# Kernel optimization log

Measured on AMD Instinct MI355X. Metric: run time of the kernel, lower is better.

## Reference

```python
import jax, jax.numpy as jnp
import numpy as np

B, T, D, H = 2, 2048, 1024, 16
DK = D // H


def setup_inputs() -> dict:
    key = jax.random.key(0)
    ks = jax.random.split(key, 9)
    s = 1.0 / np.sqrt(D)
    x = jax.random.normal(ks[0], (B, T, D), dtype=jnp.float32)
    # causal mask (1 = attend, 0 = masked), broadcast over batch and heads
    mask = jnp.tril(jnp.ones((T, T), dtype=jnp.int32))[None, None, :, :]
    Wq = jax.random.uniform(ks[1], (D, D), jnp.float32, -s, s)
    bq = jax.random.uniform(ks[2], (D,), jnp.float32, -s, s)
    Wk = jax.random.uniform(ks[3], (D, D), jnp.float32, -s, s)
    bk = jax.random.uniform(ks[4], (D,), jnp.float32, -s, s)
    Wv = jax.random.uniform(ks[5], (D, D), jnp.float32, -s, s)
    bv = jax.random.uniform(ks[6], (D,), jnp.float32, -s, s)
    Wo = jax.random.uniform(ks[7], (D, D), jnp.float32, -s, s)
    bo = jax.random.uniform(ks[8], (D,), jnp.float32, -s, s)
    return {"x": x, "mask": mask, "Wq": Wq, "bq": bq, "Wk": Wk, "bk": bk,
            "Wv": Wv, "bv": bv, "Wo": Wo, "bo": bo}


def reference(x, mask, Wq, bq, Wk, bk, Wv, bv, Wo, bo):
    # nn.Linear: y = x @ W.T + b
    q = (x @ Wq.T + bq).reshape(B, T, H, DK).transpose(0, 2, 1, 3)  # [B,H,T,DK]
    k = (x @ Wk.T + bk).reshape(B, T, H, DK).transpose(0, 2, 1, 3)
    v = (x @ Wv.T + bv).reshape(B, T, H, DK).transpose(0, 2, 1, 3)
    scores = jnp.einsum('bhqd,bhkd->bhqk', q, k) / np.sqrt(DK).astype(np.float32)
    scores = jnp.where(mask == 0, -jnp.inf, scores)
    attn = jax.nn.softmax(scores, axis=-1)
    out = jnp.einsum('bhqk,bhkd->bhqd', attn, v)  # [B,H,T,DK]
    out = out.transpose(0, 2, 1, 3).reshape(B, T, D)
    return out @ Wo.T + bo
```

## Files before the change

kernel.cpp:

```cpp
#include <hip/hip_runtime.h>

typedef unsigned short u16;
typedef unsigned long long u64;
typedef __attribute__((ext_vector_type(8))) short short8;
typedef __attribute__((ext_vector_type(4))) float f32x4;

#define B_ 2
#define T_ 2048
#define D_ 1024
#define H_ 16
#define DK_ 64

__device__ __forceinline__ u16 f2bf(float f){
  unsigned u = __float_as_uint(f);
  return (u16)((u + 0x7fffu + ((u >> 16) & 1u)) >> 16);
}

#if defined(__has_builtin)
#if __has_builtin(__builtin_amdgcn_global_load_lds)
#define HAS_GLLDS 1
#endif
#endif

#ifdef HAS_GLLDS
__device__ __forceinline__ void gl_lds16(const u16* g, u16* l){
  __builtin_amdgcn_global_load_lds(
      (__attribute__((address_space(1))) void*)(void*)g,
      (__attribute__((address_space(3))) void*)(void*)l, 16, 0, 0);
}
#endif

__global__ __launch_bounds__(256) void conv_x_k(const float* __restrict__ in,
                                                u16* __restrict__ out){
  int i = blockIdx.x * 256 + threadIdx.x;
  float4 v = ((const float4*)in)[i];
  u64 r = (u64)f2bf(v.x) | ((u64)f2bf(v.y) << 16) | ((u64)f2bf(v.z) << 32) | ((u64)f2bf(v.w) << 48);
  ((u64*)out)[i] = r;
}

__global__ __launch_bounds__(256) void conv_w_k(const float* w0, const float* w1,
                                                const float* w2, const float* w3,
                                                u16* o0, u16* o1, u16* o2, u16* o3){
  const float* src; u16* dst;
  switch (blockIdx.y){
    case 0: src = w0; dst = o0; break;
    case 1: src = w1; dst = o1; break;
    case 2: src = w2; dst = o2; break;
    default: src = w3; dst = o3; break;
  }
  int i = blockIdx.x * 256 + threadIdx.x;
  float4 v = ((const float4*)src)[i];
  u64 r = (u64)f2bf(v.x) | ((u64)f2bf(v.y) << 16) | ((u64)f2bf(v.z) << 32) | ((u64)f2bf(v.w) << 48);
  ((u64*)dst)[i] = r;
}

template<int NSEL, int OUT_F32>
__global__ __launch_bounds__(256) void gemm_bt_v2(
    const u16* __restrict__ A,
    const u16* __restrict__ W0, const u16* __restrict__ W1, const u16* __restrict__ W2,
    const float* __restrict__ b0, const float* __restrict__ b1, const float* __restrict__ b2,
    void* __restrict__ o0, void* __restrict__ o1, void* __restrict__ o2)
{
  __shared__ u16 As[128 * 32];
  __shared__ u16 Bs[128 * 32];
  const int tid = threadIdx.x;
  const int sel = (NSEL == 3) ? (blockIdx.x >> 3) : 0;
  const int n0 = (blockIdx.x & 7) * 128;
  const int m0 = blockIdx.y * 128;
  const u16* Bw = (sel == 0) ? W0 : ((sel == 1) ? W1 : W2);
  const float* bias = (sel == 0) ? b0 : ((sel == 1) ? b1 : b2);
  void* C = (sel == 0) ? o0 : ((sel == 1) ? o1 : o2);
  const int w = tid >> 6, l = tid & 63;
  const int lr = l & 15, lg = l >> 4;
  const int wm = (w & 1) * 64, wn = (w >> 1) * 64;
  f32x4 acc[4][4] = {};
  const u16* Ab = A  + (size_t)m0 * 1024;
  const u16* Bb = Bw + (size_t)n0 * 1024;
  for (int k0 = 0; k0 < 1024; k0 += 32){
    __syncthreads();
#ifdef HAS_GLLDS
#pragma unroll
    for (int i = 0; i < 2; ++i){
      int c = w * 2 + i;
      gl_lds16(Ab + (size_t)(16 * c + (l >> 2)) * 1024 + k0 + (l & 3) * 8, &As[c * 512]);
      gl_lds16(Bb + (size_t)(16 * c + (l >> 2)) * 1024 + k0 + (l & 3) * 8, &Bs[c * 512]);
    }
#else
#pragma unroll
    for (int p = 0; p < 2; ++p){
      int idx = p * 256 + tid; int row = idx >> 2; int cg = (idx & 3) * 8;
      *(uint4*)&As[row * 32 + cg] = *(const uint4*)(Ab + (size_t)row * 1024 + k0 + cg);
      *(uint4*)&Bs[row * 32 + cg] = *(const uint4*)(Bb + (size_t)row * 1024 + k0 + cg);
    }
#endif
    __syncthreads();
    short8 af[4], bfr[4];
#pragma unroll
    for (int mi = 0; mi < 4; ++mi) af[mi]  = *(const short8*)&As[(wm + 16 * mi + lr) * 32 + 8 * lg];
#pragma unroll
    for (int ni = 0; ni < 4; ++ni) bfr[ni] = *(const short8*)&Bs[(wn + 16 * ni + lr) * 32 + 8 * lg];
#pragma unroll
    for (int mi = 0; mi < 4; ++mi)
#pragma unroll
      for (int ni = 0; ni < 4; ++ni)
        acc[mi][ni] = __builtin_amdgcn_mfma_f32_16x16x32_bf16(af[mi], bfr[ni], acc[mi][ni], 0, 0, 0);
  }
  float bv[4];
#pragma unroll
  for (int ni = 0; ni < 4; ++ni) bv[ni] = bias[n0 + wn + 16 * ni + lr];
#pragma unroll
  for (int mi = 0; mi < 4; ++mi)
#pragma unroll
    for (int ni = 0; ni < 4; ++ni)
#pragma unroll
      for (int r = 0; r < 4; ++r){
        float v = acc[mi][ni][r] + bv[ni];
        size_t off = (size_t)(m0 + wm + 16 * mi + lg * 4 + r) * 1024 + (n0 + wn + 16 * ni + lr);
        if (OUT_F32) ((float*)C)[off] = v;
        else         ((u16*)C)[off]   = f2bf(v);
      }
}

__global__ __launch_bounds__(256) void transpose_v_k(const u16* __restrict__ V,
                                                     u16* __restrict__ VT){
  __shared__ u16 L[64 * 72];
  const int tid = threadIdx.x;
  const int tc = blockIdx.x, h = blockIdx.y, b = blockIdx.z;
#pragma unroll
  for (int p = 0; p < 2; ++p){
    int row = (tid >> 3) + 32 * p, g = tid & 7;
    *(uint4*)&L[row * 72 + g * 8] =
        *(const uint4*)(V + ((size_t)(b * T_ + tc * 64 + row) * H_ + h) * DK_ + g * 8);
  }
  __syncthreads();
#pragma unroll
  for (int p = 0; p < 2; ++p){
    int d = tid >> 2, g8 = (tid & 3) + 4 * p;
    union { uint4 u; u16 s[8]; } tv;
#pragma unroll
    for (int i = 0; i < 8; ++i){
      int pp = 8 * g8 + i;
      int tl = 16 * (pp & 3) + (pp >> 2);
      tv.s[i] = L[tl * 72 + d];
    }
    *(uint4*)(VT + ((size_t)(b * H_ + h) * DK_ + d) * T_ + tc * 64 + 8 * g8) = tv.u;
  }
}

#define AP 72
__global__ __launch_bounds__(256) void attn_v2(
    const u16* __restrict__ Q, const u16* __restrict__ K,
    const u16* __restrict__ VTp, u16* __restrict__ O)
{
  __shared__ u16 Ks[64 * AP];
  __shared__ u16 VTs[64 * AP];
  __shared__ u16 Ps[4][32 * AP];
  const int tid = threadIdx.x;
  const int w = tid >> 6, l = tid & 63;
  const int lr = l & 15, lg = l >> 4;
  const int h = blockIdx.y, b = blockIdx.z;
  const int qtb = (b == 0) ? blockIdx.x : (T_ / 128 - 1 - blockIdx.x);
  const int q0 = qtb * 128;
  const int wrow0 = q0 + w * 32;

  short8 qf[2][2];
#pragma unroll
  for (int mi = 0; mi < 2; ++mi)
#pragma unroll
    for (int s = 0; s < 2; ++s)
      qf[mi][s] = *(const short8*)(Q + ((size_t)(b * T_ + wrow0 + mi * 16 + lr) * H_ + h) * DK_ + s * 32 + lg * 8);

  f32x4 acc[2][4] = {};
  float lsum[2][4] = {};
  const int ktend = 2 * qtb + 1;
  const int srow = tid >> 3, sg = tid & 7;

  for (int kt = 0; kt <= ktend; ++kt){
    __syncthreads();
#pragma unroll
    for (int p = 0; p < 2; ++p){
      int row = srow + 32 * p;
      *(uint4*)&Ks[row * AP + sg * 8] =
          *(const uint4*)(K + ((size_t)(b * T_ + kt * 64 + row) * H_ + h) * DK_ + sg * 8);
      *(uint4*)&VTs[row * AP + sg * 8] =
          *(const uint4*)(VTp + ((size_t)(b * H_ + h) * DK_ + row) * T_ + kt * 64 + sg * 8);
    }
    __syncthreads();
    if (kt * 64 <= wrow0 + 31){
      short8 kf[4][2];
#pragma unroll
      for (int j0 = 0; j0 < 4; ++j0)
#pragma unroll
        for (int s = 0; s < 2; ++s)
          kf[j0][s] = *(const short8*)&Ks[(j0 * 16 + lr) * AP + s * 32 + 8 * lg];
      f32x4 sc[2][4];
#pragma unroll
      for (int mi = 0; mi < 2; ++mi)
#pragma unroll
        for (int j0 = 0; j0 < 4; ++j0){
          f32x4 z = {};
          z = __builtin_amdgcn_mfma_f32_16x16x32_bf16(qf[mi][0], kf[j0][0], z, 0, 0, 0);
          z = __builtin_amdgcn_mfma_f32_16x16x32_bf16(qf[mi][1], kf[j0][1], z, 0, 0, 0);
          sc[mi][j0] = z;
        }
      const bool domask = (kt * 64 + 63 > wrow0);
      const int kcol0 = kt * 64;
#pragma unroll
      for (int mi = 0; mi < 2; ++mi)
#pragma unroll
        for (int r = 0; r < 4; ++r){
          const int qrow = wrow0 + mi * 16 + lg * 4 + r;
          u64 pv = 0; float ls = 0.f;
#pragma unroll
          for (int j0 = 0; j0 < 4; ++j0){
            float p = __expf(sc[mi][j0][r] * 0.125f);
            if (domask && (kcol0 + j0 * 16 + lr > qrow)) p = 0.f;
            ls += p;
            pv |= ((u64)f2bf(p)) << (16 * j0);
          }
          lsum[mi][r] += ls;
          *(u64*)&Ps[w][(mi * 16 + lg * 4 + r) * AP + 4 * lr] = pv;
        }
#pragma unroll
      for (int ks = 0; ks < 2; ++ks){
        short8 pf0 = *(const short8*)&Ps[w][(lr) * AP + 32 * ks + 8 * lg];
        short8 pf1 = *(const short8*)&Ps[w][(16 + lr) * AP + 32 * ks + 8 * lg];
#pragma unroll
        for (int d0 = 0; d0 < 4; ++d0){
          short8 vf = *(const short8*)&VTs[(d0 * 16 + lr) * AP + 32 * ks + 8 * lg];
          acc[0][d0] = __builtin_amdgcn_mfma_f32_16x16x32_bf16(pf0, vf, acc[0][d0], 0, 0, 0);
          acc[1][d0] = __builtin_amdgcn_mfma_f32_16x16x32_bf16(pf1, vf, acc[1][d0], 0, 0, 0);
        }
      }
    }
  }

#pragma unroll
  for (int mi = 0; mi < 2; ++mi)
#pragma unroll
    for (int r = 0; r < 4; ++r){
      float v = lsum[mi][r];
      v += __shfl_xor(v, 1); v += __shfl_xor(v, 2);
      v += __shfl_xor(v, 4); v += __shfl_xor(v, 8);
      lsum[mi][r] = v;
    }
#pragma unroll
  for (int mi = 0; mi < 2; ++mi)
#pragma unroll
    for (int d0 = 0; d0 < 4; ++d0)
#pragma unroll
      for (int r = 0; r < 4; ++r){
        float ov = acc[mi][d0][r] / lsum[mi][r];
        O[((size_t)(b * T_ + wrow0 + mi * 16 + lg * 4 + r) * H_ + h) * DK_ + d0 * 16 + lr] = f2bf(ov);
      }
}

extern "C" void kernel_launch(void* const* d_in, const int* in_sizes, int n_in,
                              void* d_out, int out_size, void* d_ws, size_t ws_size,
                              hipStream_t stream)
{
  const float* x  = (const float*)d_in[0];
  const float* Wq = (const float*)d_in[2];
  const float* bq = (const float*)d_in[3];
  const float* Wk = (const float*)d_in[4];
  const float* bk = (const float*)d_in[5];
  const float* Wv = (const float*)d_in[6];
  const float* bv = (const float*)d_in[7];
  const float* Wo = (const float*)d_in[8];
  const float* bo = (const float*)d_in[9];

  char* ws = (char*)d_ws;
  u16* xb  = (u16*)(ws + 0);
  u16* wqb = (u16*)(ws + 8388608);
  u16* wkb = (u16*)(ws + 10485760);
  u16* wvb = (u16*)(ws + 12582912);
  u16* wob = (u16*)(ws + 14680064);
  u16* qb  = (u16*)(ws + 16777216);
  u16* kb  = (u16*)(ws + 25165824);
  u16* vb  = (u16*)(ws + 33554432);
  u16* vtb = xb;
  u16* ab  = vb;

  conv_x_k<<<4096, 256, 0, stream>>>(x, xb);
  conv_w_k<<<dim3(1024, 4), 256, 0, stream>>>(Wq, Wk, Wv, Wo, wqb, wkb, wvb, wob);

  gemm_bt_v2<3, 0><<<dim3(24, 32), 256, 0, stream>>>(
      xb, wqb, wkb, wvb, bq, bk, bv, (void*)qb, (void*)kb, (void*)vb);

  transpose_v_k<<<dim3(T_ / 64, H_, B_), 256, 0, stream>>>(vb, vtb);

  attn_v2<<<dim3(T_ / 128, H_, B_), 256, 0, stream>>>(qb, kb, vtb, ab);

  gemm_bt_v2<1, 1><<<dim3(8, 32), 256, 0, stream>>>(
      ab, wob, wob, wob, bo, bo, bo, d_out, d_out, d_out);
}
```

Measured before the change: 141.3 us.

## Double-buffer GEMM and attention tiles, swizzle K/VT, fold softmax scale into Q

Both the GEMM and the attention kernels now double-buffer their LDS tiles, so the next tile's global-to-LDS load is issued before the current tile is computed, and each loop iteration needs one barrier instead of two. K and V^T are written with an XOR swizzle so attention can use unpadded LDS tiles without bank conflicts. The softmax scale times log2(e) is folded into Q in the projection epilogue, which lets attention use exp2 and packed bf16 conversion. The conversion kernels are merged into one launch, the final division becomes a reciprocal multiply, and launch bounds are raised. The costs are more LDS per block and swizzled layouts that every producer and consumer must agree on.

```diff
diff --git a/kernel.cpp b/kernel.cpp
--- a/kernel.cpp
+++ b/kernel.cpp
@@ -1,25 +1,38 @@
 #include <hip/hip_runtime.h>
 
 typedef unsigned short u16;
+typedef unsigned int u32;
 typedef unsigned long long u64;
 typedef __attribute__((ext_vector_type(8))) short short8;
 typedef __attribute__((ext_vector_type(4))) float f32x4;
 
 #define B_ 2
 #define T_ 2048
-#define D_ 1024
 #define H_ 16
 #define DK_ 64
+#define QSCALE 0.18033688011112042f
 
 __device__ __forceinline__ u16 f2bf(float f){
   unsigned u = __float_as_uint(f);
   return (u16)((u + 0x7fffu + ((u >> 16) & 1u)) >> 16);
 }
 
+__device__ __forceinline__ u32 cvtpk(float lo, float hi){
+  u32 r;
+  asm("v_cvt_pk_bf16_f32 %0, %1, %2" : "=v"(r) : "v"(lo), "v"(hi));
+  return r;
+}
+
 #if defined(__has_builtin)
 #if __has_builtin(__builtin_amdgcn_global_load_lds)
 #define HAS_GLLDS 1
 #endif
+#if __has_builtin(__builtin_amdgcn_exp2f)
+#define EXP2(x) __builtin_amdgcn_exp2f(x)
+#endif
+#endif
+#ifndef EXP2
+#define EXP2(x) __expf(0.69314718056f * (x))
 #endif
 
 #ifdef HAS_GLLDS
@@ -30,95 +43,106 @@
 }
 #endif
 
-__global__ __launch_bounds__(256) void conv_x_k(const float* __restrict__ in,
-                                                u16* __restrict__ out){
-  int i = blockIdx.x * 256 + threadIdx.x;
-  float4 v = ((const float4*)in)[i];
-  u64 r = (u64)f2bf(v.x) | ((u64)f2bf(v.y) << 16) | ((u64)f2bf(v.z) << 32) | ((u64)f2bf(v.w) << 48);
-  ((u64*)out)[i] = r;
-}
-
-__global__ __launch_bounds__(256) void conv_w_k(const float* w0, const float* w1,
-                                                const float* w2, const float* w3,
-                                                u16* o0, u16* o1, u16* o2, u16* o3){
-  const float* src; u16* dst;
-  switch (blockIdx.y){
-    case 0: src = w0; dst = o0; break;
-    case 1: src = w1; dst = o1; break;
-    case 2: src = w2; dst = o2; break;
-    default: src = w3; dst = o3; break;
-  }
-  int i = blockIdx.x * 256 + threadIdx.x;
-  float4 v = ((const float4*)src)[i];
-  u64 r = (u64)f2bf(v.x) | ((u64)f2bf(v.y) << 16) | ((u64)f2bf(v.z) << 32) | ((u64)f2bf(v.w) << 48);
-  ((u64*)dst)[i] = r;
-}
-
-template<int NSEL, int OUT_F32>
-__global__ __launch_bounds__(256) void gemm_bt_v2(
+__global__ __launch_bounds__(256) void conv_all(
+    const float* __restrict__ x, const float* __restrict__ wq, const float* __restrict__ wk,
+    const float* __restrict__ wv, const float* __restrict__ wo,
+    u16* __restrict__ xb, u16* __restrict__ wqb, u16* __restrict__ wkb,
+    u16* __restrict__ wvb, u16* __restrict__ wob)
+{
+  int gid = blockIdx.x * 256 + threadIdx.x;
+  const float* src; u16* dst; int off;
+  if (gid < 1048576){ src = x; dst = xb; off = gid; }
+  else {
+    int t = gid - 1048576; int s = t >> 18; off = t & 262143;
+    src = (s==0)?wq:((s==1)?wk:((s==2)?wv:wo));
+    dst = (s==0)?wqb:((s==1)?wkb:((s==2)?wvb:wob));
+  }
+  float4 v = ((const float4*)src)[off];
+  u64 r = (u64)f2bf(v.x) | ((u64)f2bf(v.y)<<16) | ((u64)f2bf(v.z)<<32) | ((u64)f2bf(v.w)<<48);
+  ((u64*)dst)[off] = r;
+}
+
+template<int QKV>
+__global__ __launch_bounds__(256, 3) void gemm_k3(
     const u16* __restrict__ A,
     const u16* __restrict__ W0, const u16* __restrict__ W1, const u16* __restrict__ W2,
     const float* __restrict__ b0, const float* __restrict__ b1, const float* __restrict__ b2,
     void* __restrict__ o0, void* __restrict__ o1, void* __restrict__ o2)
 {
-  __shared__ u16 As[128 * 32];
-  __shared__ u16 Bs[128 * 32];
+  __shared__ u16 As[2][128*32];
+  __shared__ u16 Bs[2][128*32];
   const int tid = threadIdx.x;
-  const int sel = (NSEL == 3) ? (blockIdx.x >> 3) : 0;
+  const int sel = QKV ? (blockIdx.x >> 3) : 0;
   const int n0 = (blockIdx.x & 7) * 128;
   const int m0 = blockIdx.y * 128;
-  const u16* Bw = (sel == 0) ? W0 : ((sel == 1) ? W1 : W2);
-  const float* bias = (sel == 0) ? b0 : ((sel == 1) ? b1 : b2);
-  void* C = (sel == 0) ? o0 : ((sel == 1) ? o1 : o2);
-  const int w = tid >> 6, l = tid & 63;
-  const int lr = l & 15, lg = l >> 4;
-  const int wm = (w & 1) * 64, wn = (w >> 1) * 64;
+  const u16* Bw = (sel==0)?W0:((sel==1)?W1:W2);
+  const float* bias = (sel==0)?b0:((sel==1)?b1:b2);
+  const int w = tid>>6, l = tid&63;
+  const int lr = l&15, lg = l>>4;
+  const int wm = (w&1)*64, wn = (w>>1)*64;
+  const u16* Ab = A  + (size_t)m0*1024 + (size_t)(l>>2)*1024 + (l&3)*8;
+  const u16* Bb = Bw + (size_t)n0*1024 + (size_t)(l>>2)*1024 + (l&3)*8;
   f32x4 acc[4][4] = {};
-  const u16* Ab = A  + (size_t)m0 * 1024;
-  const u16* Bb = Bw + (size_t)n0 * 1024;
-  for (int k0 = 0; k0 < 1024; k0 += 32){
+
+#define G_STAGE(k0, pb) do {                                                    \
+    _Pragma("unroll")                                                           \
+    for (int i_ = 0; i_ < 2; ++i_){                                             \
+      int c_ = w*2 + i_;                                                        \
+      G_STAGE_ONE(Ab, As, c_, k0, pb); G_STAGE_ONE(Bb, Bs, c_, k0, pb);         \
+    } } while(0)
+#ifdef HAS_GLLDS
+#define G_STAGE_ONE(SRC, DST, c_, k0, pb) \
+    gl_lds16(SRC + (size_t)(16*(c_))*1024 + (k0), &DST[pb][(c_)*512])
+#else
+#define G_STAGE_ONE(SRC, DST, c_, k0, pb) \
+    *(uint4*)&DST[pb][(c_)*512 + l*8] = *(const uint4*)(SRC + (size_t)(16*(c_))*1024 + (k0))
+#endif
+
+  G_STAGE(0, 0);
+  __syncthreads();
+  for (int it = 0; it < 32; ++it){
+    const int pb = it & 1;
+    if (it < 31) G_STAGE((it+1)*32, pb^1);
+    short8 af[4], bf[4];
+#pragma unroll
+    for (int mi=0;mi<4;++mi) af[mi] = *(const short8*)&As[pb][(wm+16*mi+lr)*32 + 8*lg];
+#pragma unroll
+    for (int ni=0;ni<4;++ni) bf[ni] = *(const short8*)&Bs[pb][(wn+16*ni+lr)*32 + 8*lg];
+#pragma unroll
+    for (int mi=0;mi<4;++mi)
+#pragma unroll
+      for (int ni=0;ni<4;++ni)
+        acc[mi][ni] = __builtin_amdgcn_mfma_f32_16x16x32_bf16(af[mi], bf[ni], acc[mi][ni], 0,0,0);
     __syncthreads();
-#ifdef HAS_GLLDS
-#pragma unroll
-    for (int i = 0; i < 2; ++i){
-      int c = w * 2 + i;
-      gl_lds16(Ab + (size_t)(16 * c + (l >> 2)) * 1024 + k0 + (l & 3) * 8, &As[c * 512]);
-      gl_lds16(Bb + (size_t)(16 * c + (l >> 2)) * 1024 + k0 + (l & 3) * 8, &Bs[c * 512]);
+  }
+
+  float bv[4];
+#pragma unroll
+  for (int ni=0;ni<4;++ni) bv[ni] = bias[n0+wn+16*ni+lr];
+  void* C = QKV ? ((sel==0)?o0:((sel==1)?o1:o2)) : o0;
+#pragma unroll
+  for (int mi=0;mi<4;++mi)
+#pragma unroll
+    for (int r=0;r<4;++r){
+      const int trow = m0 + wm + 16*mi + 4*lg + r;
+#pragma unroll
+      for (int ni=0;ni<4;++ni){
+        float v = acc[mi][ni][r] + bv[ni];
+        int n = n0 + wn + 16*ni + lr;
+        if (!QKV){
+          ((float*)C)[(size_t)trow*1024 + n] = v;
+        } else if (sel == 0){
+          ((u16*)C)[(size_t)trow*1024 + n] = f2bf(v * QSCALE);
+        } else if (sel == 1){
+          int nsw = (n & ~63) | ((n & 63) ^ ((trow & 7) << 3));
+          ((u16*)C)[(size_t)trow*1024 + nsw] = f2bf(v);
+        } else {
+          ((u16*)C)[(size_t)trow*1024 + n] = f2bf(v);
+        }
+      }
     }
-#else
-#pragma unroll
-    for (int p = 0; p < 2; ++p){
-      int idx = p * 256 + tid; int row = idx >> 2; int cg = (idx & 3) * 8;
-      *(uint4*)&As[row * 32 + cg] = *(const uint4*)(Ab + (size_t)row * 1024 + k0 + cg);
-      *(uint4*)&Bs[row * 32 + cg] = *(const uint4*)(Bb + (size_t)row * 1024 + k0 + cg);
-    }
-#endif
-    __syncthreads();
-    short8 af[4], bfr[4];
-#pragma unroll
-    for (int mi = 0; mi < 4; ++mi) af[mi]  = *(const short8*)&As[(wm + 16 * mi + lr) * 32 + 8 * lg];
-#pragma unroll
-    for (int ni = 0; ni < 4; ++ni) bfr[ni] = *(const short8*)&Bs[(wn + 16 * ni + lr) * 32 + 8 * lg];
-#pragma unroll
-    for (int mi = 0; mi < 4; ++mi)
-#pragma unroll
-      for (int ni = 0; ni < 4; ++ni)
-        acc[mi][ni] = __builtin_amdgcn_mfma_f32_16x16x32_bf16(af[mi], bfr[ni], acc[mi][ni], 0, 0, 0);
-  }
-  float bv[4];
-#pragma unroll
-  for (int ni = 0; ni < 4; ++ni) bv[ni] = bias[n0 + wn + 16 * ni + lr];
-#pragma unroll
-  for (int mi = 0; mi < 4; ++mi)
-#pragma unroll
-    for (int ni = 0; ni < 4; ++ni)
-#pragma unroll
-      for (int r = 0; r < 4; ++r){
-        float v = acc[mi][ni][r] + bv[ni];
-        size_t off = (size_t)(m0 + wm + 16 * mi + lg * 4 + r) * 1024 + (n0 + wn + 16 * ni + lr);
-        if (OUT_F32) ((float*)C)[off] = v;
-        else         ((u16*)C)[off]   = f2bf(v);
-      }
+#undef G_STAGE
+#undef G_STAGE_ONE
 }
 
 __global__ __launch_bounds__(256) void transpose_v_k(const u16* __restrict__ V,
@@ -143,116 +167,135 @@
       int tl = 16 * (pp & 3) + (pp >> 2);
       tv.s[i] = L[tl * 72 + d];
     }
-    *(uint4*)(VT + ((size_t)(b * H_ + h) * DK_ + d) * T_ + tc * 64 + 8 * g8) = tv.u;
-  }
-}
-
-#define AP 72
-__global__ __launch_bounds__(256) void attn_v2(
+    *(uint4*)(VT + ((size_t)(b * H_ + h) * DK_ + d) * T_ + tc * 64 + ((8 * g8) ^ ((d & 7) << 3))) = tv.u;
+  }
+}
+
+__global__ __launch_bounds__(256, 2) void attn_v3(
     const u16* __restrict__ Q, const u16* __restrict__ K,
-    const u16* __restrict__ VTp, u16* __restrict__ O)
+    const u16* __restrict__ VT, u16* __restrict__ O)
 {
-  __shared__ u16 Ks[64 * AP];
-  __shared__ u16 VTs[64 * AP];
-  __shared__ u16 Ps[4][32 * AP];
+  __shared__ u16 Ks[2][64*64];
+  __shared__ u16 VTs[2][64*64];
+  __shared__ u16 Ps[4][32*72];
   const int tid = threadIdx.x;
-  const int w = tid >> 6, l = tid & 63;
-  const int lr = l & 15, lg = l >> 4;
+  const int w = tid>>6, l = tid&63;
+  const int lr = l&15, lg = l>>4;
   const int h = blockIdx.y, b = blockIdx.z;
-  const int qtb = (b == 0) ? blockIdx.x : (T_ / 128 - 1 - blockIdx.x);
+  const int qtb = (b==0) ? blockIdx.x : (15 - blockIdx.x);
   const int q0 = qtb * 128;
-  const int wrow0 = q0 + w * 32;
+  const int wrow0 = q0 + w*32;
+  const int sl_r = l>>3, sl_c = (l&7)*8;
+  const size_t kbase = ((size_t)(b*T_) * H_ + h) * DK_;
+  const size_t vbase = (size_t)(b*H_ + h) * DK_ * (size_t)T_;
+
+#define A_STAGE(kt, pb) do {                                                       \
+    _Pragma("unroll")                                                              \
+    for (int p_=0;p_<2;++p_){                                                      \
+      int r0_ = 8*w + 32*p_;                                                       \
+      A_STAGE_K(kt, pb, r0_); A_STAGE_V(kt, pb, r0_);                              \
+    } } while(0)
+#ifdef HAS_GLLDS
+#define A_STAGE_K(kt, pb, r0_) \
+    gl_lds16(K  + kbase + (size_t)((kt)*64 + r0_ + sl_r)*1024 + sl_c, &Ks[pb][r0_*64])
+#define A_STAGE_V(kt, pb, r0_) \
+    gl_lds16(VT + vbase + (size_t)(r0_ + sl_r)*T_ + (kt)*64 + sl_c, &VTs[pb][r0_*64])
+#else
+#define A_STAGE_K(kt, pb, r0_) \
+    *(uint4*)&Ks[pb][(r0_+sl_r)*64 + sl_c] = *(const uint4*)(K + kbase + (size_t)((kt)*64 + r0_ + sl_r)*1024 + sl_c)
+#define A_STAGE_V(kt, pb, r0_) \
+    *(uint4*)&VTs[pb][(r0_+sl_r)*64 + sl_c] = *(const uint4*)(VT + vbase + (size_t)(r0_ + sl_r)*T_ + (kt)*64 + sl_c)
+#endif
 
   short8 qf[2][2];
 #pragma unroll
-  for (int mi = 0; mi < 2; ++mi)
-#pragma unroll
-    for (int s = 0; s < 2; ++s)
-      qf[mi][s] = *(const short8*)(Q + ((size_t)(b * T_ + wrow0 + mi * 16 + lr) * H_ + h) * DK_ + s * 32 + lg * 8);
+  for (int mi=0;mi<2;++mi)
+#pragma unroll
+    for (int s=0;s<2;++s)
+      qf[mi][s] = *(const short8*)(Q + kbase + (size_t)(wrow0 + 16*mi + lr)*1024 + s*32 + 8*lg);
 
   f32x4 acc[2][4] = {};
   float lsum[2][4] = {};
-  const int ktend = 2 * qtb + 1;
-  const int srow = tid >> 3, sg = tid & 7;
-
+  const int ktend = 2*qtb + 1;
+
+  A_STAGE(0, 0);
+  __syncthreads();
   for (int kt = 0; kt <= ktend; ++kt){
-    __syncthreads();
-#pragma unroll
-    for (int p = 0; p < 2; ++p){
-      int row = srow + 32 * p;
-      *(uint4*)&Ks[row * AP + sg * 8] =
-          *(const uint4*)(K + ((size_t)(b * T_ + kt * 64 + row) * H_ + h) * DK_ + sg * 8);
-      *(uint4*)&VTs[row * AP + sg * 8] =
-          *(const uint4*)(VTp + ((size_t)(b * H_ + h) * DK_ + row) * T_ + kt * 64 + sg * 8);
-    }
-    __syncthreads();
-    if (kt * 64 <= wrow0 + 31){
+    const int pb = kt & 1;
+    if (kt < ktend) A_STAGE(kt+1, pb^1);
+    if (kt*64 <= wrow0 + 31){
       short8 kf[4][2];
 #pragma unroll
-      for (int j0 = 0; j0 < 4; ++j0)
-#pragma unroll
-        for (int s = 0; s < 2; ++s)
-          kf[j0][s] = *(const short8*)&Ks[(j0 * 16 + lr) * AP + s * 32 + 8 * lg];
+      for (int j0=0;j0<4;++j0)
+#pragma unroll
+        for (int s=0;s<2;++s)
+          kf[j0][s] = *(const short8*)&Ks[pb][(j0*16+lr)*64 + (((4*s+lg) ^ (lr&7))<<3)];
       f32x4 sc[2][4];
 #pragma unroll
-      for (int mi = 0; mi < 2; ++mi)
-#pragma unroll
-        for (int j0 = 0; j0 < 4; ++j0){
+      for (int mi=0;mi<2;++mi)
+#pragma unroll
+        for (int j0=0;j0<4;++j0){
           f32x4 z = {};
-          z = __builtin_amdgcn_mfma_f32_16x16x32_bf16(qf[mi][0], kf[j0][0], z, 0, 0, 0);
-          z = __builtin_amdgcn_mfma_f32_16x16x32_bf16(qf[mi][1], kf[j0][1], z, 0, 0, 0);
+          z = __builtin_amdgcn_mfma_f32_16x16x32_bf16(qf[mi][0], kf[j0][0], z, 0,0,0);
+          z = __builtin_amdgcn_mfma_f32_16x16x32_bf16(qf[mi][1], kf[j0][1], z, 0,0,0);
           sc[mi][j0] = z;
         }
-      const bool domask = (kt * 64 + 63 > wrow0);
-      const int kcol0 = kt * 64;
-#pragma unroll
-      for (int mi = 0; mi < 2; ++mi)
-#pragma unroll
-        for (int r = 0; r < 4; ++r){
-          const int qrow = wrow0 + mi * 16 + lg * 4 + r;
-          u64 pv = 0; float ls = 0.f;
-#pragma unroll
-          for (int j0 = 0; j0 < 4; ++j0){
-            float p = __expf(sc[mi][j0][r] * 0.125f);
-            if (domask && (kcol0 + j0 * 16 + lr > qrow)) p = 0.f;
-            ls += p;
-            pv |= ((u64)f2bf(p)) << (16 * j0);
+      const bool diag = (kt*64 + 63 > wrow0);
+#pragma unroll
+      for (int mi=0;mi<2;++mi)
+#pragma unroll
+        for (int r=0;r<4;++r){
+          float p0,p1,p2,p3;
+          if (diag){
+            const int lim = wrow0 + 16*mi + 4*lg + r - kt*64;
+            p0 = (lr      <= lim) ? EXP2(sc[mi][0][r]) : 0.f;
+            p1 = (16+lr   <= lim) ? EXP2(sc[mi][1][r]) : 0.f;
+            p2 = (32+lr   <= lim) ? EXP2(sc[mi][2][r]) : 0.f;
+            p3 = (48+lr   <= lim) ? EXP2(sc[mi][3][r]) : 0.f;
+          } else {
+            p0 = EXP2(sc[mi][0][r]); p1 = EXP2(sc[mi][1][r]);
+            p2 = EXP2(sc[mi][2][r]); p3 = EXP2(sc[mi][3][r]);
           }
-          lsum[mi][r] += ls;
-          *(u64*)&Ps[w][(mi * 16 + lg * 4 + r) * AP + 4 * lr] = pv;
+          lsum[mi][r] += (p0+p1)+(p2+p3);
+          u64 pv = (u64)cvtpk(p0,p1) | ((u64)cvtpk(p2,p3) << 32);
+          *(u64*)&Ps[w][(16*mi+4*lg+r)*72 + 4*lr] = pv;
         }
 #pragma unroll
-      for (int ks = 0; ks < 2; ++ks){
-        short8 pf0 = *(const short8*)&Ps[w][(lr) * AP + 32 * ks + 8 * lg];
-        short8 pf1 = *(const short8*)&Ps[w][(16 + lr) * AP + 32 * ks + 8 * lg];
-#pragma unroll
-        for (int d0 = 0; d0 < 4; ++d0){
-          short8 vf = *(const short8*)&VTs[(d0 * 16 + lr) * AP + 32 * ks + 8 * lg];
-          acc[0][d0] = __builtin_amdgcn_mfma_f32_16x16x32_bf16(pf0, vf, acc[0][d0], 0, 0, 0);
-          acc[1][d0] = __builtin_amdgcn_mfma_f32_16x16x32_bf16(pf1, vf, acc[1][d0], 0, 0, 0);
+      for (int ks=0;ks<2;++ks){
+        short8 pf0 = *(const short8*)&Ps[w][lr*72      + 32*ks + 8*lg];
+        short8 pf1 = *(const short8*)&Ps[w][(16+lr)*72 + 32*ks + 8*lg];
+#pragma unroll
+        for (int d0=0;d0<4;++d0){
+          short8 vf = *(const short8*)&VTs[pb][(d0*16+lr)*64 + (((4*ks+lg) ^ (lr&7))<<3)];
+          acc[0][d0] = __builtin_amdgcn_mfma_f32_16x16x32_bf16(pf0, vf, acc[0][d0], 0,0,0);
+          acc[1][d0] = __builtin_amdgcn_mfma_f32_16x16x32_bf16(pf1, vf, acc[1][d0], 0,0,0);
         }
       }
     }
-  }
-
-#pragma unroll
-  for (int mi = 0; mi < 2; ++mi)
-#pragma unroll
-    for (int r = 0; r < 4; ++r){
+    __syncthreads();
+  }
+
+#pragma unroll
+  for (int mi=0;mi<2;++mi)
+#pragma unroll
+    for (int r=0;r<4;++r){
       float v = lsum[mi][r];
-      v += __shfl_xor(v, 1); v += __shfl_xor(v, 2);
-      v += __shfl_xor(v, 4); v += __shfl_xor(v, 8);
-      lsum[mi][r] = v;
+      v += __shfl_xor(v,1); v += __shfl_xor(v,2);
+      v += __shfl_xor(v,4); v += __shfl_xor(v,8);
+      lsum[mi][r] = 1.0f / v;
     }
 #pragma unroll
-  for (int mi = 0; mi < 2; ++mi)
-#pragma unroll
-    for (int d0 = 0; d0 < 4; ++d0)
-#pragma unroll
-      for (int r = 0; r < 4; ++r){
-        float ov = acc[mi][d0][r] / lsum[mi][r];
-        O[((size_t)(b * T_ + wrow0 + mi * 16 + lg * 4 + r) * H_ + h) * DK_ + d0 * 16 + lr] = f2bf(ov);
+  for (int mi=0;mi<2;++mi)
+#pragma unroll
+    for (int d0=0;d0<4;++d0)
+#pragma unroll
+      for (int r=0;r<4;++r){
+        float ov = acc[mi][d0][r] * lsum[mi][r];
+        O[kbase + (size_t)(wrow0 + 16*mi + 4*lg + r)*1024 + d0*16 + lr] = f2bf(ov);
       }
+#undef A_STAGE
+#undef A_STAGE_K
+#undef A_STAGE_V
 }
 
 extern "C" void kernel_launch(void* const* d_in, const int* in_sizes, int n_in,
@@ -281,16 +324,15 @@
   u16* vtb = xb;
   u16* ab  = vb;
 
-  conv_x_k<<<4096, 256, 0, stream>>>(x, xb);
-  conv_w_k<<<dim3(1024, 4), 256, 0, stream>>>(Wq, Wk, Wv, Wo, wqb, wkb, wvb, wob);
-
-  gemm_bt_v2<3, 0><<<dim3(24, 32), 256, 0, stream>>>(
+  conv_all<<<8192, 256, 0, stream>>>(x, Wq, Wk, Wv, Wo, xb, wqb, wkb, wvb, wob);
+
+  gemm_k3<1><<<dim3(24, 32), 256, 0, stream>>>(
       xb, wqb, wkb, wvb, bq, bk, bv, (void*)qb, (void*)kb, (void*)vb);
 
-  transpose_v_k<<<dim3(T_ / 64, H_, B_), 256, 0, stream>>>(vb, vtb);
-
-  attn_v2<<<dim3(T_ / 128, H_, B_), 256, 0, stream>>>(qb, kb, vtb, ab);
-
-  gemm_bt_v2<1, 1><<<dim3(8, 32), 256, 0, stream>>>(
+  transpose_v_k<<<dim3(T_/64, H_, B_), 256, 0, stream>>>(vb, vtb);
+
+  attn_v3<<<dim3(T_/128, H_, B_), 256, 0, stream>>>(qb, kb, vtb, ab);
+
+  gemm_k3<0><<<dim3(8, 32), 256, 0, stream>>>(
       ab, wob, wob, wob, bo, bo, bo, d_out, d_out, d_out);
 }
```

After: 126.3 us. -10.6%, faster.
